# Kernel tuning notes

Measured on AMD Instinct MI355X. Metric: run time of the kernel, lower is better.

Reference implementation:

```python
import jax, jax.numpy as jnp
import numpy as np

B, N, C, M = 2048, 1024, 128, 64


def setup_inputs() -> dict:
    key = jax.random.key(0)
    k1, k2, k3 = jax.random.split(key, 3)
    src = jax.random.normal(k1, (B, N, C), dtype=jnp.float32)
    tar = jax.random.normal(k2, (B, M, C), dtype=jnp.float32)
    indices = jax.random.randint(k3, (B, M), 0, N, dtype=jnp.int32)
    return {"src": src, "tar": tar, "indices": indices}


def reference(src, tar, indices):
    # Erase-add gate (DKVMN write): for each batch, zero the memory rows
    # listed in `indices`, then scatter-add the target features into them.
    def per_batch(s, t, idx):
        # s: (N, C), t: (M, C), idx: (M,)
        erase_mask = jnp.zeros((s.shape[0], 1), s.dtype).at[idx].set(1.0)  # (N,1)
        erased = s * (1.0 - erase_mask)
        return erased.at[idx].add(t)  # duplicates accumulate, like index_add

    return jax.vmap(per_batch)(src, tar, indices)
```

## Files before the change

kernel.cpp:

```cpp
#include <hip/hip_runtime.h>

constexpr int kB  = 2048;
constexpr int kN  = 1024;
constexpr int kC  = 128;
constexpr int kM  = 64;
constexpr int kC4 = kC / 4;

constexpr int RPB = 64;
constexpr int BPB = kN / RPB;
constexpr int ITEMS = RPB * kC4 / 256;

__global__ __launch_bounds__(256) void eag_fused(const float4* __restrict__ src,
                                                 const float4* __restrict__ tar,
                                                 const int* __restrict__ indices,
                                                 float4* __restrict__ out) {
    const int bid  = blockIdx.x;
    const int b    = bid >> 4;
    const int row0 = (bid & (BPB - 1)) * RPB;
    const int tid  = threadIdx.x;

    __shared__ int idx[kM];
    __shared__ int flag[RPB];

    if (tid < kM) {
        idx[tid]  = indices[b * kM + tid];
        flag[tid] = 0;
    }
    __syncthreads();
    if (tid < kM) {
        const int rel = idx[tid] - row0;
        if (rel >= 0 && rel < RPB) flag[rel] = 1;
    }

    const long long base = ((long long)b * kN + row0) * kC4;
    float4 v[ITEMS];
#pragma unroll
    for (int k = 0; k < ITEMS; ++k) {
        v[k] = src[base + tid + k * 256];
    }

    __syncthreads();

    const float4* tb = tar + (long long)b * kM * kC4;
#pragma unroll
    for (int k = 0; k < ITEMS; ++k) {
        const int w = tid + k * 256;
        const int r = w >> 5;
        if (flag[r]) {
            const int c4 = w & (kC4 - 1);
            const int n  = row0 + r;
            float4 acc = {0.f, 0.f, 0.f, 0.f};
            for (int m = 0; m < kM; ++m) {
                if (idx[m] == n) {
                    const float4 t = tb[m * kC4 + c4];
                    acc.x += t.x; acc.y += t.y; acc.z += t.z; acc.w += t.w;
                }
            }
            v[k] = acc;
        }
    }

#pragma unroll
    for (int k = 0; k < ITEMS; ++k) {
        out[base + tid + k * 256] = v[k];
    }
}

extern "C" void kernel_launch(void* const* d_in, const int* in_sizes, int n_in,
                              void* d_out, int out_size, void* d_ws, size_t ws_size,
                              hipStream_t stream) {
    const float4* src     = (const float4*)d_in[0];
    const float4* tar     = (const float4*)d_in[1];
    const int*    indices = (const int*)d_in[2];
    float4*       out     = (float4*)d_out;

    eag_fused<<<kB * BPB, 256, 0, stream>>>(src, tar, indices, out);
}
```

Before: 429.8 us.

## Replace shared-memory flags with wave ballot/shuffle and use nontemporal loads/stores

Removes the shared-memory index and flag arrays and both block barriers. Each wavefront now loads the 64 indices, one per lane, builds a ballot mask of indices falling in this block's row range, and walks only those set bits with shuffles to find matching rows. Source loads and output stores switch to nontemporal builtins so the streaming traffic bypasses cache retention. The catch is that every thread now loops over the masked indices instead of checking a per-row flag, which adds some ALU work.

New measurement: 430.3 us. Within noise of the previous version (+0.1%).

```diff
diff --git a/kernel.cpp b/kernel.cpp
--- a/kernel.cpp
+++ b/kernel.cpp
@@ -6,73 +6,64 @@
 constexpr int kM  = 64;
 constexpr int kC4 = kC / 4;
 
-constexpr int RPB = 64;
-constexpr int BPB = kN / RPB;
+constexpr int RPB   = 64;
+constexpr int BPB   = kN / RPB;
 constexpr int ITEMS = RPB * kC4 / 256;
 
-__global__ __launch_bounds__(256) void eag_fused(const float4* __restrict__ src,
-                                                 const float4* __restrict__ tar,
+using f4 = __attribute__((ext_vector_type(4))) float;
+
+__global__ __launch_bounds__(256) void eag_fused(const f4* __restrict__ src,
+                                                 const f4* __restrict__ tar,
                                                  const int* __restrict__ indices,
-                                                 float4* __restrict__ out) {
+                                                 f4* __restrict__ out) {
     const int bid  = blockIdx.x;
     const int b    = bid >> 4;
     const int row0 = (bid & (BPB - 1)) * RPB;
     const int tid  = threadIdx.x;
+    const int lane = tid & 63;
 
-    __shared__ int idx[kM];
-    __shared__ int flag[RPB];
-
-    if (tid < kM) {
-        idx[tid]  = indices[b * kM + tid];
-        flag[tid] = 0;
-    }
-    __syncthreads();
-    if (tid < kM) {
-        const int rel = idx[tid] - row0;
-        if (rel >= 0 && rel < RPB) flag[rel] = 1;
+    const long long base = ((long long)b * kN + row0) * kC4;
+    f4 v[ITEMS];
+#pragma unroll
+    for (int k = 0; k < ITEMS; ++k) {
+        v[k] = __builtin_nontemporal_load(src + base + tid + k * 256);
     }
 
-    const long long base = ((long long)b * kN + row0) * kC4;
-    float4 v[ITEMS];
+    const int my_idx = indices[b * kM + lane];
+    const int rel    = my_idx - row0;
+    const unsigned long long mask = __ballot(rel >= 0 && rel < RPB);
+
+    const f4* tb = tar + (long long)b * kM * kC4;
+    const int c4 = tid & (kC4 - 1);
 #pragma unroll
     for (int k = 0; k < ITEMS; ++k) {
-        v[k] = src[base + tid + k * 256];
-    }
-
-    __syncthreads();
-
-    const float4* tb = tar + (long long)b * kM * kC4;
-#pragma unroll
-    for (int k = 0; k < ITEMS; ++k) {
-        const int w = tid + k * 256;
-        const int r = w >> 5;
-        if (flag[r]) {
-            const int c4 = w & (kC4 - 1);
-            const int n  = row0 + r;
-            float4 acc = {0.f, 0.f, 0.f, 0.f};
-            for (int m = 0; m < kM; ++m) {
-                if (idx[m] == n) {
-                    const float4 t = tb[m * kC4 + c4];
-                    acc.x += t.x; acc.y += t.y; acc.z += t.z; acc.w += t.w;
-                }
+        const int n = row0 + ((tid + k * 256) >> 5);
+        f4 acc = {0.f, 0.f, 0.f, 0.f};
+        bool hit = false;
+        for (unsigned long long mm = mask; mm; mm &= mm - 1) {
+            const int m = (int)__builtin_ctzll(mm);
+            const int t = __shfl(my_idx, m);
+            if (t == n) {
+                hit = true;
+                acc += tb[m * kC4 + c4];
             }
-            v[k] = acc;
         }
+        if (hit) v[k] = acc;
     }
 
 #pragma unroll
     for (int k = 0; k < ITEMS; ++k) {
-        out[base + tid + k * 256] = v[k];
+        __builtin_nontemporal_store(v[k], out + base + tid + k * 256);
     }
 }
 
 extern "C" void kernel_launch(void* const* d_in, const int* in_sizes, int n_in,
                               void* d_out, int out_size, void* d_ws, size_t ws_size,
                               hipStream_t stream) {
-    const float4* src     = (const float4*)d_in[0];
-    const float4* tar     = (const float4*)d_in[1];
-    const int*    indices = (const int*)d_in[2];
-    float4*       out     = (float4*)d_out;
+    const f4*  src     = (const f4*)d_in[0];
+    const f4*  tar     = (const f4*)d_in[1];
+    const int* indices = (const int*)d_in[2];
+    f4*        out     = (f4*)d_out;
 
     eag_fused<<<kB * BPB, 256, 0, stream>>>(src, tar, indices, out);
 }
```
